# Performance work log

Measured on AMD Instinct MI355X. Metric: run time of the kernel, lower is better.

## Reference

```python
import jax, jax.numpy as jnp
import numpy as np

B, S, D, H = 4, 2048, 768, 12
HD = D // H  # head_dim = 64
NEG = 1e10
EPS = 1e-5

def setup_inputs() -> dict:
    key = jax.random.key(0)
    k1, k2, k3 = jax.random.split(key, 3)
    return {
        "context": jax.random.normal(k1, (B, S, D), dtype=jnp.float32),
        "pad_mask": jnp.ones((B, S), dtype=jnp.float32),
        "w_qkv": jax.random.normal(k2, (D, 3 * D), dtype=jnp.float32) * 0.02,
        "w_proj": jax.random.normal(k3, (D, D), dtype=jnp.float32) * (0.02 / np.sqrt(2.0 * 12)),
        "b_proj": jnp.zeros((D,), dtype=jnp.float32),
        "gamma": jnp.ones((D,), dtype=jnp.float32),
        "beta": jnp.zeros((D,), dtype=jnp.float32),
    }

def reference(context, pad_mask, w_qkv, w_proj, b_proj, gamma, beta):
    b, s, d = context.shape
    resid = context
    qkv = context @ w_qkv                       # [B,S,3D]
    q, k, v = jnp.split(qkv, 3, axis=-1)
    # [B,S,D] -> [B,H,S,HD]
    q = q.reshape(b, s, H, HD).transpose(0, 2, 1, 3)
    k = k.reshape(b, s, H, HD).transpose(0, 2, 1, 3)
    v = v.reshape(b, s, H, HD).transpose(0, 2, 1, 3)
    scores = jnp.einsum("bhqd,bhkd->bhqk", q, k) * (1.0 / np.sqrt(HD))
    m = pad_mask[:, None, None, :]              # [B,1,1,S]
    scores = scores * m - (1.0 - m) * NEG       # multiplicative mask + big negative
    attn = jax.nn.softmax(scores, axis=-1)      # dropout is identity at inference
    out = jnp.einsum("bhqk,bhkd->bhqd", attn, v)
    out = out.transpose(0, 2, 1, 3).reshape(b, s, d)
    out = out @ w_proj + b_proj
    x = out + resid
    mu = jnp.mean(x, axis=-1, keepdims=True)
    var = jnp.var(x, axis=-1, keepdims=True)
    return (x - mu) * jax.lax.rsqrt(var + EPS) * gamma + beta
```

## Files before the change

### kernel.cpp

```cpp
#include <hip/hip_runtime.h>

#define BB 4
#define SS 2048
#define DD 768
#define HH 12
#define HDD 64
#define BS (BB*SS)
#define NQKV (3*DD)
#define NEL (BS*DD)

#define NB_PACK 6144
#define NB_TQKV 1728
#define NB_TPRJ 576

typedef __attribute__((ext_vector_type(8))) __bf16 bf16x8;
typedef __attribute__((ext_vector_type(4))) float fx4;
typedef __attribute__((ext_vector_type(4))) int   ix4;

#define MFMA16(a,b,c) __builtin_amdgcn_mfma_f32_16x16x32_bf16((a),(b),(c),0,0,0)

__device__ __forceinline__ unsigned short f2bf(float f) {
  unsigned u = __builtin_bit_cast(unsigned, f);
  u = (u + 0x7FFFu + ((u >> 16) & 1u)) >> 16;
  return (unsigned short)u;
}
__device__ __forceinline__ unsigned pkbf(float a, float b) {
  unsigned ua = __builtin_bit_cast(unsigned, a);
  unsigned ub = __builtin_bit_cast(unsigned, b);
  return ((ua + 0x8000u) >> 16) | ((ub + 0x8000u) & 0xFFFF0000u);
}

__global__ __launch_bounds__(256) void prep_k(const float* __restrict__ ctx,
                                              unsigned short* __restrict__ Xbf,
                                              const float* __restrict__ wqkv,
                                              unsigned short* __restrict__ WqkvT,
                                              const float* __restrict__ wproj,
                                              unsigned short* __restrict__ WprojT) {
  const int bid = blockIdx.x;
  const int tid = threadIdx.x;
  if (bid < NB_PACK) {
    int i = bid * 256 + tid;
    float4 v = ((const float4*)ctx)[i];
    ((uint2*)Xbf)[i] = make_uint2(pkbf(v.x, v.y), pkbf(v.z, v.w));
    return;
  }
  __shared__ unsigned short t[32][33];
  const float* w; unsigned short* wT; int N, bx, by;
  if (bid < NB_PACK + NB_TQKV) {
    int b2 = bid - NB_PACK;
    w = wqkv; wT = WqkvT; N = NQKV; bx = b2 % 72; by = b2 / 72;
  } else {
    int b3 = bid - NB_PACK - NB_TQKV;
    w = wproj; wT = WprojT; N = DD; bx = b3 % 24; by = b3 / 24;
  }
  int n0 = bx * 32, k0 = by * 32;
  int tx = tid & 31, ty = tid >> 5;
#pragma unroll
  for (int r = ty; r < 32; r += 8)
    t[tx][r] = f2bf(w[(size_t)(k0 + r) * N + n0 + tx]);
  __syncthreads();
#pragma unroll
  for (int r = ty; r < 32; r += 8)
    wT[(size_t)(n0 + r) * DD + k0 + tx] = t[r][tx];
}

__global__ __launch_bounds__(256) void gemm_qkv_k(const unsigned short* __restrict__ Wt,
                                                  const unsigned short* __restrict__ X,
                                                  unsigned short* __restrict__ Qo,
                                                  unsigned short* __restrict__ Ko,
                                                  unsigned short* __restrict__ Vto) {
  __shared__ unsigned short As[2][128 * 32];
  __shared__ unsigned short Bs[2][128 * 32];
  const int tid = threadIdx.x;
  const int w = tid >> 6, lane = tid & 63, quad = lane >> 4, l16 = lane & 15;
  const int m0 = blockIdx.y << 7;
  const int n0 = blockIdx.x << 7;
  const int wm = (w & 1) * 64, wn = (w >> 1) * 64;
  fx4 acc[4][4];
#pragma unroll
  for (int i = 0; i < 4; ++i)
#pragma unroll
    for (int c = 0; c < 4; ++c) acc[i][c] = (fx4){0.f, 0.f, 0.f, 0.f};

  const int c0 = tid, c1 = 256 + tid;
  const unsigned short* Ag0 = Wt + (size_t)(m0 + (c0 >> 2)) * DD + (c0 & 3) * 8;
  const unsigned short* Ag1 = Wt + (size_t)(m0 + (c1 >> 2)) * DD + (c1 & 3) * 8;
  const unsigned short* Bg0 = X + (size_t)(n0 + (c0 >> 2)) * DD + (c0 & 3) * 8;
  const unsigned short* Bg1 = X + (size_t)(n0 + (c1 >> 2)) * DD + (c1 & 3) * 8;

  ix4 ra0 = *(const ix4*)Ag0;
  ix4 ra1 = *(const ix4*)Ag1;
  ix4 rb0 = *(const ix4*)Bg0;
  ix4 rb1 = *(const ix4*)Bg1;
  *(ix4*)((char*)As[0] + c0 * 16) = ra0;
  *(ix4*)((char*)As[0] + c1 * 16) = ra1;
  *(ix4*)((char*)Bs[0] + c0 * 16) = rb0;
  *(ix4*)((char*)Bs[0] + c1 * 16) = rb1;
  __syncthreads();

  for (int k0 = 0; k0 < DD; k0 += 32) {
    const int cur = (k0 >> 5) & 1;
    const bool more = (k0 + 32 < DD);
    if (more) {
      ra0 = *(const ix4*)(Ag0 + k0 + 32);
      ra1 = *(const ix4*)(Ag1 + k0 + 32);
      rb0 = *(const ix4*)(Bg0 + k0 + 32);
      rb1 = *(const ix4*)(Bg1 + k0 + 32);
    }
    bf16x8 af[4], bf[4];
#pragma unroll
    for (int i = 0; i < 4; ++i) af[i] = *(const bf16x8*)&As[cur][(wm + i * 16 + l16) * 32 + quad * 8];
#pragma unroll
    for (int c = 0; c < 4; ++c) bf[c] = *(const bf16x8*)&Bs[cur][(wn + c * 16 + l16) * 32 + quad * 8];
#pragma unroll
    for (int i = 0; i < 4; ++i)
#pragma unroll
      for (int c = 0; c < 4; ++c) acc[i][c] = MFMA16(af[i], bf[c], acc[i][c]);
    if (more) {
      *(ix4*)((char*)As[cur ^ 1] + c0 * 16) = ra0;
      *(ix4*)((char*)As[cur ^ 1] + c1 * 16) = ra1;
      *(ix4*)((char*)Bs[cur ^ 1] + c0 * 16) = rb0;
      *(ix4*)((char*)Bs[cur ^ 1] + c1 * 16) = rb1;
    }
    __syncthreads();
  }

  const int which = m0 / DD;
#pragma unroll
  for (int i = 0; i < 4; ++i) {
    int fb = m0 + wm + i * 16 + quad * 4;
    int d = fb - which * DD;
    int h = d >> 6, hd = d & 63;
#pragma unroll
    for (int c = 0; c < 4; ++c) {
      int srow = n0 + wn + c * 16 + l16;
      int b = srow >> 11, s = srow & (SS - 1);
      if (which == 0) {
        uint2 v = make_uint2(pkbf(acc[i][c][0], acc[i][c][1]), pkbf(acc[i][c][2], acc[i][c][3]));
        *(uint2*)&Qo[((size_t)(b * HH + h) * SS + s) * HDD + hd] = v;
      } else if (which == 1) {
        uint2 v = make_uint2(pkbf(acc[i][c][0], acc[i][c][1]), pkbf(acc[i][c][2], acc[i][c][3]));
        *(uint2*)&Ko[((size_t)(b * HH + h) * SS + s) * HDD + hd] = v;
      } else {
#pragma unroll
        for (int r = 0; r < 4; ++r)
          Vto[((size_t)(b * HH + h) * HDD + hd + r) * SS + s] = f2bf(acc[i][c][r]);
      }
    }
  }
}

__global__ __launch_bounds__(256) void gemm_proj_k(const unsigned short* __restrict__ Wt,
                                                   const unsigned short* __restrict__ X,
                                                   const float* __restrict__ ctx,
                                                   const float* __restrict__ bproj,
                                                   float* __restrict__ xf) {
  __shared__ unsigned short As[2][128 * 32];
  __shared__ unsigned short Bs[2][128 * 32];
  const int tid = threadIdx.x;
  const int w = tid >> 6, lane = tid & 63, quad = lane >> 4, l16 = lane & 15;
  const int m0 = blockIdx.y << 7;
  const int n0 = blockIdx.x << 7;
  const int wm = (w & 1) * 64, wn = (w >> 1) * 64;
  fx4 acc[4][4];
#pragma unroll
  for (int i = 0; i < 4; ++i)
#pragma unroll
    for (int c = 0; c < 4; ++c) acc[i][c] = (fx4){0.f, 0.f, 0.f, 0.f};

  const int c0 = tid, c1 = 256 + tid;
  const unsigned short* Ag0 = Wt + (size_t)(m0 + (c0 >> 2)) * DD + (c0 & 3) * 8;
  const unsigned short* Ag1 = Wt + (size_t)(m0 + (c1 >> 2)) * DD + (c1 & 3) * 8;
  const unsigned short* Bg0 = X + (size_t)(n0 + (c0 >> 2)) * DD + (c0 & 3) * 8;
  const unsigned short* Bg1 = X + (size_t)(n0 + (c1 >> 2)) * DD + (c1 & 3) * 8;

  ix4 ra0 = *(const ix4*)Ag0;
  ix4 ra1 = *(const ix4*)Ag1;
  ix4 rb0 = *(const ix4*)Bg0;
  ix4 rb1 = *(const ix4*)Bg1;
  *(ix4*)((char*)As[0] + c0 * 16) = ra0;
  *(ix4*)((char*)As[0] + c1 * 16) = ra1;
  *(ix4*)((char*)Bs[0] + c0 * 16) = rb0;
  *(ix4*)((char*)Bs[0] + c1 * 16) = rb1;
  __syncthreads();

  for (int k0 = 0; k0 < DD; k0 += 32) {
    const int cur = (k0 >> 5) & 1;
    const bool more = (k0 + 32 < DD);
    if (more) {
      ra0 = *(const ix4*)(Ag0 + k0 + 32);
      ra1 = *(const ix4*)(Ag1 + k0 + 32);
      rb0 = *(const ix4*)(Bg0 + k0 + 32);
      rb1 = *(const ix4*)(Bg1 + k0 + 32);
    }
    bf16x8 af[4], bf[4];
#pragma unroll
    for (int i = 0; i < 4; ++i) af[i] = *(const bf16x8*)&As[cur][(wm + i * 16 + l16) * 32 + quad * 8];
#pragma unroll
    for (int c = 0; c < 4; ++c) bf[c] = *(const bf16x8*)&Bs[cur][(wn + c * 16 + l16) * 32 + quad * 8];
#pragma unroll
    for (int i = 0; i < 4; ++i)
#pragma unroll
      for (int c = 0; c < 4; ++c) acc[i][c] = MFMA16(af[i], bf[c], acc[i][c]);
    if (more) {
      *(ix4*)((char*)As[cur ^ 1] + c0 * 16) = ra0;
      *(ix4*)((char*)As[cur ^ 1] + c1 * 16) = ra1;
      *(ix4*)((char*)Bs[cur ^ 1] + c0 * 16) = rb0;
      *(ix4*)((char*)Bs[cur ^ 1] + c1 * 16) = rb1;
    }
    __syncthreads();
  }

#pragma unroll
  for (int i = 0; i < 4; ++i) {
    int fb = m0 + wm + i * 16 + quad * 4;
    float4 bp = *(const float4*)&bproj[fb];
#pragma unroll
    for (int c = 0; c < 4; ++c) {
      int srow = n0 + wn + c * 16 + l16;
      float4 cx = *(const float4*)&ctx[(size_t)srow * DD + fb];
      float4 r;
      r.x = acc[i][c][0] + bp.x + cx.x;
      r.y = acc[i][c][1] + bp.y + cx.y;
      r.z = acc[i][c][2] + bp.z + cx.z;
      r.w = acc[i][c][3] + bp.w + cx.w;
      *(float4*)&xf[(size_t)srow * DD + fb] = r;
    }
  }
}

__global__ __launch_bounds__(256) void attn_k(const unsigned short* __restrict__ Q,
                                              const unsigned short* __restrict__ K,
                                              const unsigned short* __restrict__ Vt,
                                              const float* __restrict__ mask,
                                              unsigned short* __restrict__ O) {
  __shared__ unsigned short Ks[2][64 * 64];
  __shared__ unsigned short Vts[2][64 * 64];
  const int tid = threadIdx.x;
  const int w = tid >> 6, lane = tid & 63;
  const int quad = lane >> 4, l16 = lane & 15;
  const int bh = blockIdx.y;
  const int b = bh / HH, h = bh - b * HH;
  const int q0 = blockIdx.x << 7;
  const unsigned short* Qb = Q + (size_t)bh * (SS * HDD);
  const unsigned short* Kb = K + (size_t)bh * (SS * HDD);
  const unsigned short* Vtb = Vt + (size_t)bh * (SS * HDD);
  const float* mb = mask + b * SS;

  const float C2 = 0.125f * 1.44269504089f;
  const float OFF2 = 1.0e10f * 1.44269504089f;

  bf16x8 qf[2][2];
#pragma unroll
  for (int qi = 0; qi < 2; ++qi)
#pragma unroll
    for (int f = 0; f < 2; ++f)
      qf[qi][f] = *(const bf16x8*)&Qb[(size_t)(q0 + w * 32 + qi * 16 + l16) * HDD + f * 32 + quad * 8];

  fx4 o[2][4];
#pragma unroll
  for (int qi = 0; qi < 2; ++qi)
#pragma unroll
    for (int ht = 0; ht < 4; ++ht) o[qi][ht] = (fx4){0.f, 0.f, 0.f, 0.f};
  float lsum[2] = {0.f, 0.f};

  const int cA = tid, cB = 256 + tid;
  const int rA = cA >> 3, pA = (cA & 7) ^ (rA & 7);
  const int rB = cB >> 3, pB = (cB & 7) ^ (rB & 7);

  ix4 rk0 = *(const ix4*)&Kb[(size_t)rA * HDD + pA * 8];
  ix4 rk1 = *(const ix4*)&Kb[(size_t)rB * HDD + pB * 8];
  ix4 rv0 = *(const ix4*)&Vtb[(size_t)rA * SS + pA * 8];
  ix4 rv1 = *(const ix4*)&Vtb[(size_t)rB * SS + pB * 8];
  *(ix4*)((char*)Ks[0] + cA * 16) = rk0;
  *(ix4*)((char*)Ks[0] + cB * 16) = rk1;
  *(ix4*)((char*)Vts[0] + cA * 16) = rv0;
  *(ix4*)((char*)Vts[0] + cB * 16) = rv1;
  __syncthreads();

  for (int k0 = 0; k0 < SS; k0 += 64) {
    const int cur = (k0 >> 6) & 1;
    const bool more = (k0 + 64 < SS);
    if (more) {
      int kn = k0 + 64;
      rk0 = *(const ix4*)&Kb[(size_t)(kn + rA) * HDD + pA * 8];
      rk1 = *(const ix4*)&Kb[(size_t)(kn + rB) * HDD + pB * 8];
      rv0 = *(const ix4*)&Vtb[(size_t)rA * SS + kn + pA * 8];
      rv1 = *(const ix4*)&Vtb[(size_t)rB * SS + kn + pB * 8];
    }
    const unsigned short* KsC = Ks[cur];
    const unsigned short* VtsC = Vts[cur];

    float4 offn[4];
#pragma unroll
    for (int kt = 0; kt < 4; ++kt) {
      float4 mv = *(const float4*)&mb[k0 + kt * 16 + quad * 4];
      offn[kt].x = fmaf(OFF2, mv.x, -OFF2);
      offn[kt].y = fmaf(OFF2, mv.y, -OFF2);
      offn[kt].z = fmaf(OFF2, mv.z, -OFF2);
      offn[kt].w = fmaf(OFF2, mv.w, -OFF2);
    }

    bf16x8 kf[4][2];
#pragma unroll
    for (int kt = 0; kt < 4; ++kt) {
      int row = kt * 16 + l16;
      int rx = row & 7;
#pragma unroll
      for (int f = 0; f < 2; ++f)
        kf[kt][f] = *(const bf16x8*)&KsC[row * 64 + ((f * 4 + quad) ^ rx) * 8];
    }
    bf16x8 vf[4][2];
#pragma unroll
    for (int ht = 0; ht < 4; ++ht) {
      int row = ht * 16 + l16;
      int rx = row & 7;
#pragma unroll
      for (int f = 0; f < 2; ++f) {
        int dc0 = (f * 4 + (quad >> 1)) ^ rx;
        int dc1 = (f * 4 + 2 + (quad >> 1)) ^ rx;
        uint2 lo = *(const uint2*)((const char*)VtsC + row * 128 + dc0 * 16 + (quad & 1) * 8);
        uint2 hi = *(const uint2*)((const char*)VtsC + row * 128 + dc1 * 16 + (quad & 1) * 8);
        ix4 vv = (ix4){(int)lo.x, (int)lo.y, (int)hi.x, (int)hi.y};
        vf[ht][f] = __builtin_bit_cast(bf16x8, vv);
      }
    }

#pragma unroll
    for (int qi = 0; qi < 2; ++qi) {
      fx4 sc[4];
#pragma unroll
      for (int kt = 0; kt < 4; ++kt) {
        fx4 s = (fx4){0.f, 0.f, 0.f, 0.f};
        s = MFMA16(kf[kt][0], qf[qi][0], s);
        s = MFMA16(kf[kt][1], qf[qi][1], s);
        sc[kt] = s;
      }
      unsigned pk[4][2];
      float ls = 0.f;
#pragma unroll
      for (int kt = 0; kt < 4; ++kt) {
        const float* offr = (const float*)&offn[kt];
        float p[4];
#pragma unroll
        for (int r = 0; r < 4; ++r)
          p[r] = exp2f(fmaf(sc[kt][r], C2, offr[r]));
        ls += (p[0] + p[1]) + (p[2] + p[3]);
        pk[kt][0] = pkbf(p[0], p[1]);
        pk[kt][1] = pkbf(p[2], p[3]);
      }
      lsum[qi] += ls;
      ix4 p0 = (ix4){(int)pk[0][0], (int)pk[0][1], (int)pk[1][0], (int)pk[1][1]};
      ix4 p1 = (ix4){(int)pk[2][0], (int)pk[2][1], (int)pk[3][0], (int)pk[3][1]};
      bf16x8 pf0 = __builtin_bit_cast(bf16x8, p0);
      bf16x8 pf1 = __builtin_bit_cast(bf16x8, p1);
#pragma unroll
      for (int ht = 0; ht < 4; ++ht) {
        o[qi][ht] = MFMA16(vf[ht][0], pf0, o[qi][ht]);
        o[qi][ht] = MFMA16(vf[ht][1], pf1, o[qi][ht]);
      }
    }

    if (more) {
      *(ix4*)((char*)Ks[cur ^ 1] + cA * 16) = rk0;
      *(ix4*)((char*)Ks[cur ^ 1] + cB * 16) = rk1;
      *(ix4*)((char*)Vts[cur ^ 1] + cA * 16) = rv0;
      *(ix4*)((char*)Vts[cur ^ 1] + cB * 16) = rv1;
    }
    __syncthreads();
  }

#pragma unroll
  for (int qi = 0; qi < 2; ++qi) {
    float t = lsum[qi];
    t += __shfl_xor(t, 16);
    t += __shfl_xor(t, 32);
    float inv = 1.f / fmaxf(t, 1e-30f);
    int sq = q0 + w * 32 + qi * 16 + l16;
    unsigned short* orow = O + ((size_t)(b * SS + sq)) * DD + h * HDD;
#pragma unroll
    for (int ht = 0; ht < 4; ++ht) {
      uint2 v = make_uint2(pkbf(o[qi][ht][0] * inv, o[qi][ht][1] * inv),
                           pkbf(o[qi][ht][2] * inv, o[qi][ht][3] * inv));
      *(uint2*)&orow[ht * 16 + quad * 4] = v;
    }
  }
}

__global__ __launch_bounds__(256) void ln_k(const float* __restrict__ x,
                                            const float* __restrict__ gamma,
                                            const float* __restrict__ beta,
                                            float* __restrict__ out) {
  const int row = blockIdx.x;
  const float* xr = x + (size_t)row * DD;
  const int t = threadIdx.x;
  float v0 = xr[t], v1 = xr[t + 256], v2 = xr[t + 512];
  float s = v0 + v1 + v2;
  float ss = v0 * v0 + v1 * v1 + v2 * v2;
#pragma unroll
  for (int d = 32; d > 0; d >>= 1) {
    s += __shfl_down(s, d);
    ss += __shfl_down(ss, d);
  }
  __shared__ float sh[10];
  int wv = t >> 6, lane = t & 63;
  if (lane == 0) { sh[wv] = s; sh[4 + wv] = ss; }
  __syncthreads();
  if (t == 0) {
    float S = sh[0] + sh[1] + sh[2] + sh[3];
    float SSm = sh[4] + sh[5] + sh[6] + sh[7];
    float mu = S * (1.0f / DD);
    float var = SSm * (1.0f / DD) - mu * mu;
    sh[8] = mu;
    sh[9] = rsqrtf(var + 1e-5f);
  }
  __syncthreads();
  float mu = sh[8], rstd = sh[9];
  out[(size_t)row * DD + t]       = (v0 - mu) * rstd * gamma[t]       + beta[t];
  out[(size_t)row * DD + t + 256] = (v1 - mu) * rstd * gamma[t + 256] + beta[t + 256];
  out[(size_t)row * DD + t + 512] = (v2 - mu) * rstd * gamma[t + 512] + beta[t + 512];
}

extern "C" void kernel_launch(void* const* d_in, const int* in_sizes, int n_in,
                              void* d_out, int out_size, void* d_ws, size_t ws_size,
                              hipStream_t stream) {
  (void)in_sizes; (void)n_in; (void)out_size; (void)ws_size;
  const float* ctx   = (const float*)d_in[0];
  const float* mask  = (const float*)d_in[1];
  const float* wqkv  = (const float*)d_in[2];
  const float* wproj = (const float*)d_in[3];
  const float* bproj = (const float*)d_in[4];
  const float* gamma = (const float*)d_in[5];
  const float* beta  = (const float*)d_in[6];
  float* out = (float*)d_out;

  char* p = (char*)d_ws;
  unsigned short* Xbf = (unsigned short*)p; p += (size_t)NEL * 2;
  unsigned short* Qw  = (unsigned short*)p; p += (size_t)NEL * 2;
  unsigned short* Kw  = (unsigned short*)p; p += (size_t)NEL * 2;
  unsigned short* Vtw = (unsigned short*)p; p += (size_t)NEL * 2;
  unsigned short* Ao  = (unsigned short*)p; p += (size_t)NEL * 2;
  unsigned short* WqkvT  = (unsigned short*)p; p += (size_t)DD * NQKV * 2;
  unsigned short* WprojT = (unsigned short*)p; p += (size_t)DD * DD * 2;
  float* xf = (float*)Qw;

  prep_k<<<NB_PACK + NB_TQKV + NB_TPRJ, 256, 0, stream>>>(ctx, Xbf, wqkv, WqkvT, wproj, WprojT);
  gemm_qkv_k<<<dim3(BS / 128, NQKV / 128), 256, 0, stream>>>(WqkvT, Xbf, Qw, Kw, Vtw);
  attn_k<<<dim3(SS / 128, BB * HH), 256, 0, stream>>>(Qw, Kw, Vtw, mask, Ao);
  gemm_proj_k<<<dim3(BS / 128, DD / 128), 256, 0, stream>>>(WprojT, Ao, ctx, bproj, xf);
  ln_k<<<BS, 256, 0, stream>>>(xf, gamma, beta, out);
}
```

Before: 279.9 us.

## Remap attention blocks per XCD and single-buffer K/V LDS tiles

Attention launch is flattened to a 1D grid, and block ids are remapped so that all query tiles of one batch-head land on the same XCD (block id mod 8). This lets them share K/V through that die's L2. The double-buffered LDS staging is replaced by a single buffer with two barriers per iteration, while the next tile is still prefetched into registers. This halves LDS use, which may raise occupancy, but adds an extra barrier each iteration and exposes the LDS store latency.

Result: no change. 281.1 us (+0.4%).

```diff
diff --git a/kernel.cpp b/kernel.cpp
--- a/kernel.cpp
+++ b/kernel.cpp
@@ -234,14 +234,16 @@
                                               const unsigned short* __restrict__ Vt,
                                               const float* __restrict__ mask,
                                               unsigned short* __restrict__ O) {
-  __shared__ unsigned short Ks[2][64 * 64];
-  __shared__ unsigned short Vts[2][64 * 64];
+  __shared__ unsigned short Ks[64 * 64];
+  __shared__ unsigned short Vts[64 * 64];
   const int tid = threadIdx.x;
   const int w = tid >> 6, lane = tid & 63;
   const int quad = lane >> 4, l16 = lane & 15;
-  const int bh = blockIdx.y;
+  const int bid = blockIdx.x;
+  const int xcd = bid & 7, j = bid >> 3;
+  const int bh = xcd + 8 * (j >> 4);
+  const int q0 = (j & 15) << 7;
   const int b = bh / HH, h = bh - b * HH;
-  const int q0 = blockIdx.x << 7;
   const unsigned short* Qb = Q + (size_t)bh * (SS * HDD);
   const unsigned short* Kb = K + (size_t)bh * (SS * HDD);
   const unsigned short* Vtb = Vt + (size_t)bh * (SS * HDD);
@@ -272,24 +274,21 @@
   ix4 rk1 = *(const ix4*)&Kb[(size_t)rB * HDD + pB * 8];
   ix4 rv0 = *(const ix4*)&Vtb[(size_t)rA * SS + pA * 8];
   ix4 rv1 = *(const ix4*)&Vtb[(size_t)rB * SS + pB * 8];
-  *(ix4*)((char*)Ks[0] + cA * 16) = rk0;
-  *(ix4*)((char*)Ks[0] + cB * 16) = rk1;
-  *(ix4*)((char*)Vts[0] + cA * 16) = rv0;
-  *(ix4*)((char*)Vts[0] + cB * 16) = rv1;
-  __syncthreads();
 
   for (int k0 = 0; k0 < SS; k0 += 64) {
-    const int cur = (k0 >> 6) & 1;
-    const bool more = (k0 + 64 < SS);
-    if (more) {
+    __syncthreads();
+    *(ix4*)((char*)Ks + cA * 16) = rk0;
+    *(ix4*)((char*)Ks + cB * 16) = rk1;
+    *(ix4*)((char*)Vts + cA * 16) = rv0;
+    *(ix4*)((char*)Vts + cB * 16) = rv1;
+    __syncthreads();
+    if (k0 + 64 < SS) {
       int kn = k0 + 64;
       rk0 = *(const ix4*)&Kb[(size_t)(kn + rA) * HDD + pA * 8];
       rk1 = *(const ix4*)&Kb[(size_t)(kn + rB) * HDD + pB * 8];
       rv0 = *(const ix4*)&Vtb[(size_t)rA * SS + kn + pA * 8];
       rv1 = *(const ix4*)&Vtb[(size_t)rB * SS + kn + pB * 8];
     }
-    const unsigned short* KsC = Ks[cur];
-    const unsigned short* VtsC = Vts[cur];
 
     float4 offn[4];
 #pragma unroll
@@ -308,7 +307,7 @@
       int rx = row & 7;
 #pragma unroll
       for (int f = 0; f < 2; ++f)
-        kf[kt][f] = *(const bf16x8*)&KsC[row * 64 + ((f * 4 + quad) ^ rx) * 8];
+        kf[kt][f] = *(const bf16x8*)&Ks[row * 64 + ((f * 4 + quad) ^ rx) * 8];
     }
     bf16x8 vf[4][2];
 #pragma unroll
@@ -319,8 +318,8 @@
       for (int f = 0; f < 2; ++f) {
         int dc0 = (f * 4 + (quad >> 1)) ^ rx;
         int dc1 = (f * 4 + 2 + (quad >> 1)) ^ rx;
-        uint2 lo = *(const uint2*)((const char*)VtsC + row * 128 + dc0 * 16 + (quad & 1) * 8);
-        uint2 hi = *(const uint2*)((const char*)VtsC + row * 128 + dc1 * 16 + (quad & 1) * 8);
+        uint2 lo = *(const uint2*)((const char*)Vts + row * 128 + dc0 * 16 + (quad & 1) * 8);
+        uint2 hi = *(const uint2*)((const char*)Vts + row * 128 + dc1 * 16 + (quad & 1) * 8);
         ix4 vv = (ix4){(int)lo.x, (int)lo.y, (int)hi.x, (int)hi.y};
         vf[ht][f] = __builtin_bit_cast(bf16x8, vv);
       }
@@ -360,14 +359,6 @@
         o[qi][ht] = MFMA16(vf[ht][1], pf1, o[qi][ht]);
       }
     }
-
-    if (more) {
-      *(ix4*)((char*)Ks[cur ^ 1] + cA * 16) = rk0;
-      *(ix4*)((char*)Ks[cur ^ 1] + cB * 16) = rk1;
-      *(ix4*)((char*)Vts[cur ^ 1] + cA * 16) = rv0;
-      *(ix4*)((char*)Vts[cur ^ 1] + cB * 16) = rv1;
-    }
-    __syncthreads();
   }
 
 #pragma unroll
@@ -446,7 +437,7 @@
 
   prep_k<<<NB_PACK + NB_TQKV + NB_TPRJ, 256, 0, stream>>>(ctx, Xbf, wqkv, WqkvT, wproj, WprojT);
   gemm_qkv_k<<<dim3(BS / 128, NQKV / 128), 256, 0, stream>>>(WqkvT, Xbf, Qw, Kw, Vtw);
-  attn_k<<<dim3(SS / 128, BB * HH), 256, 0, stream>>>(Qw, Kw, Vtw, mask, Ao);
+  attn_k<<<SS / 128 * BB * HH, 256, 0, stream>>>(Qw, Kw, Vtw, mask, Ao);
   gemm_proj_k<<<dim3(BS / 128, DD / 128), 256, 0, stream>>>(WprojT, Ao, ctx, bproj, xf);
   ln_k<<<BS, 256, 0, stream>>>(xf, gamma, beta, out);
 }
```
